# Optimization experiments

Measured on AMD Instinct MI355X. Metric: run time of the kernel, lower is better.

## Reference

```python
import jax, jax.numpy as jnp
import numpy as np
import math

B, S, D, H = 4, 1024, 1024, 16
HD = D // H  # 64
DFF = 4 * D
LN_EPS = 1e-5

def setup_inputs() -> dict:
    key = jax.random.key(0)
    ks = jax.random.split(key, 24)
    sd = lambda fi, fo: 1.0 / math.sqrt(fi)
    def lin(k, fi, fo):
        k1, k2 = jax.random.split(k)
        w = jax.random.uniform(k1, (fi, fo), jnp.float32, -sd(fi, fo), sd(fi, fo))
        b = jax.random.uniform(k2, (fo,), jnp.float32, -sd(fi, fo), sd(fi, fo))
        return w, b
    x = jax.random.normal(ks[0], (B, S, D), jnp.float32)
    Wk, bk = lin(ks[1], D, D)
    Wq, bq = lin(ks[2], D, D)
    Wv, bv = lin(ks[3], D, D)
    # per-head projections stacked over heads: [H, D, HD]
    def head_lin(k):
        kk = jax.random.split(k, H)
        ws, bs = zip(*[lin(kk[h], D, HD) for h in range(H)])
        return jnp.stack(ws), jnp.stack(bs)
    Whq, bhq = head_lin(ks[4])
    Whk, bhk = head_lin(ks[5])
    Whv, bhv = head_lin(ks[6])
    Wo, bo = lin(ks[7], D, D)
    W1, b1 = lin(ks[8], D, DFF)
    W2, b2 = lin(ks[9], DFF, D)
    gamma = jnp.ones((D,), jnp.float32)
    beta = jnp.zeros((D,), jnp.float32)
    return dict(x=x, Wk=Wk, bk=bk, Wq=Wq, bq=bq, Wv=Wv, bv=bv,
                Whq=Whq, bhq=bhq, Whk=Whk, bhk=bhk, Whv=Whv, bhv=bhv,
                Wo=Wo, bo=bo, W1=W1, b1=b1, W2=W2, b2=b2,
                gamma=gamma, beta=beta)

def _layer_norm(x, gamma, beta):
    mu = jnp.mean(x, axis=-1, keepdims=True)
    var = jnp.mean(jnp.square(x - mu), axis=-1, keepdims=True)
    return (x - mu) * jax.lax.rsqrt(var + LN_EPS) * gamma + beta

def reference(x, Wk, bk, Wq, bq, Wv, bv, Whq, bhq, Whk, bhk, Whv, bhv,
              Wo, bo, W1, b1, W2, b2, gamma, beta):
    # outer projections; NOTE: forward passes (k, q, v) into MHA, so the
    # MHA 'Q' stream is k_proj(x), 'K' stream is q_proj(x), 'V' is v_proj(x)
    ko = x @ Wk + bk
    qo = x @ Wq + bq
    vo = x @ Wv + bv
    # per-head projections (batched over heads): [B,H,S,HD]
    q = jnp.einsum('bsd,hde->bhse', ko, Whq) + bhq[None, :, None, :]
    k = jnp.einsum('bsd,hde->bhse', qo, Whk) + bhk[None, :, None, :]
    v = jnp.einsum('bsd,hde->bhse', vo, Whv) + bhv[None, :, None, :]
    # NOTE: original scales by sqrt(d_model), not sqrt(head_dim)
    scores = jnp.einsum('bhse,bhte->bhst', q, k) / math.sqrt(D)
    w = jax.nn.softmax(scores, axis=-1)
    o = jnp.einsum('bhst,bhte->bhse', w, v)         # [B,H,S,HD]
    o = o.transpose(0, 2, 1, 3).reshape(B, S, D)    # concat heads
    attn = o @ Wo + bo
    # dropout is identity in eval; shared LayerNorm after both residuals
    r1 = _layer_norm(x + attn, gamma, beta)
    ff = jax.nn.gelu(r1 @ W1 + b1, approximate=False) @ W2 + b2
    out = _layer_norm(r1 + ff, gamma, beta)
    return out
```

## Files before the change

### kernel.cpp

```cpp
#include <hip/hip_runtime.h>
#include <cstdint>
#include <cstddef>

#define D_MODEL 1024
#define SEQ 1024
#define BATCH 4
#define NHEAD 16
#define HDIM 64
#define ROWS (BATCH*SEQ)

typedef unsigned short u16;
typedef __attribute__((ext_vector_type(4))) unsigned short u16x4;
typedef __attribute__((ext_vector_type(8))) unsigned short u16x8;
typedef __attribute__((ext_vector_type(8))) __bf16 bf16x8v;
typedef __attribute__((ext_vector_type(4))) float f32x4;

__device__ inline u16 f2bf(float f){
  union{float f; unsigned u;} c; c.f = f;
  unsigned r = c.u + 0x7FFFu + ((c.u>>16)&1u);
  return (u16)(r>>16);
}
__device__ inline float bf2f(u16 s){
  union{unsigned u; float f;} c; c.u = ((unsigned)s)<<16; return c.f;
}
__device__ inline float gelu_f(float x){ return 0.5f*x*(1.f+erff(x*0.7071067811865475f)); }

__device__ __forceinline__ void gload_lds16(const void* g, void* l){
  __builtin_amdgcn_global_load_lds(
    (const __attribute__((address_space(1))) unsigned int*)g,
    (__attribute__((address_space(3))) unsigned int*)l, 16, 0, 0);
}

__global__ __launch_bounds__(256) void convert_bf(const float* __restrict__ in, u16* __restrict__ out){
  size_t idx = (size_t)blockIdx.x*256 + threadIdx.x;
  f32x4 v = *(const f32x4*)(in + idx*4);
  u16x4 o = { f2bf(v.x), f2bf(v.y), f2bf(v.z), f2bf(v.w) };
  *(u16x4*)(out + idx*4) = o;
}

__global__ __launch_bounds__(256) void transpose_conv(const float* __restrict__ W, u16* __restrict__ WT, int K, int N){
  __shared__ float tile[32][33];
  int n0 = blockIdx.x*32, k0 = blockIdx.y*32;
  int tx = threadIdx.x & 31, ty = threadIdx.x >> 5;
  #pragma unroll
  for (int i=0;i<4;i++){
    int r = ty + i*8;
    tile[r][tx] = W[(size_t)(k0+r)*N + n0 + tx];
  }
  __syncthreads();
  #pragma unroll
  for (int i=0;i<4;i++){
    int r = ty + i*8;
    WT[(size_t)(n0+r)*K + k0 + tx] = f2bf(tile[tx][r]);
  }
}

__global__ __launch_bounds__(256) void head_transpose(const float* __restrict__ Wh, u16* __restrict__ WT){
  __shared__ float tile[32][33];
  int d0 = blockIdx.x*32, e0 = blockIdx.y*32, h = blockIdx.z;
  int tx = threadIdx.x & 31, ty = threadIdx.x >> 5;
  #pragma unroll
  for (int i=0;i<4;i++){
    int r = ty + i*8;
    tile[r][tx] = Wh[(size_t)h*D_MODEL*HDIM + (size_t)(d0+r)*HDIM + e0 + tx];
  }
  __syncthreads();
  #pragma unroll
  for (int i=0;i<4;i++){
    int r = ty + i*8;
    WT[(size_t)(h*HDIM + e0 + r)*D_MODEL + d0 + tx] = f2bf(tile[tx][r]);
  }
}

__global__ __launch_bounds__(256) void bias_cat(const float* a, const float* b, const float* c, float* o){
  int i = blockIdx.x*256 + threadIdx.x;
  float v = (i < 1024) ? a[i] : (i < 2048) ? b[i-1024] : c[i-2048];
  o[i] = v;
}

__device__ __forceinline__ void stage128(u16 (*As)[4096], u16 (*Bs)[4096], int b,
  const u16* Ab, const u16* Bb, int Kstride, int kt, int wid, int rr, int sch)
{
  #pragma unroll
  for (int c=0;c<2;c++){
    int reg = c*4 + wid;
    int row = reg*16 + rr;
    gload_lds16(Ab + (size_t)row*Kstride + kt*32 + sch*8, &As[b][reg*512]);
  }
  #pragma unroll
  for (int c=0;c<2;c++){
    int reg = c*4 + wid;
    int row = reg*16 + rr;
    gload_lds16(Bb + (size_t)row*Kstride + kt*32 + sch*8, &Bs[b][reg*512]);
  }
}

__device__ __forceinline__ void gemm128_core(u16 (*As)[4096], u16 (*Bs)[4096],
  const u16* __restrict__ A, const u16* __restrict__ BT, const float* __restrict__ bias,
  float* __restrict__ outF, u16* __restrict__ outB,
  int N, int Kstride, int kofs, int Ksub, int mode, int act, int addbias)
{
  int t = threadIdx.x, lane = t&63, wid = t>>6;
  int wr = wid>>1, wc = wid&1;
  int fr = lane&15, kg = lane>>4;
  int gx = gridDim.x;
  int bid = blockIdx.y*gx + blockIdx.x;
  int nwg = gx*gridDim.y;
  int cpx = nwg >> 3;
  int sw = (bid&7)*cpx + (bid>>3);
  int tc = sw % gx, tr = sw / gx;

  const u16* Ab = A  + (size_t)tr*128*Kstride + kofs;
  const u16* Bb = BT + (size_t)tc*128*Kstride + kofs;
  int rr = lane>>2, cc = lane&3;
  int sch = cc ^ ((rr>>1)&3);

  f32x4 acc[4][4];
  #pragma unroll
  for (int m=0;m<4;m++)
    #pragma unroll
    for (int n=0;n<4;n++) acc[m][n] = (f32x4)0.f;

  int NT = Ksub >> 5;

  stage128(As, Bs, 0, Ab, Bb, Kstride, 0, wid, rr, sch);
  stage128(As, Bs, 1, Ab, Bb, Kstride, 1, wid, rr, sch);
  int buf = 0;
  for (int kt=0; kt<NT; ++kt){
    if (kt+2 < NT){
      int nb = buf+2; if (nb>=3) nb-=3;
      stage128(As, Bs, nb, Ab, Bb, Kstride, kt+2, wid, rr, sch);
      asm volatile("s_waitcnt vmcnt(8)" ::: "memory");
    } else if (kt+1 < NT){
      asm volatile("s_waitcnt vmcnt(4)" ::: "memory");
    } else {
      asm volatile("s_waitcnt vmcnt(0)" ::: "memory");
    }
    asm volatile("s_barrier" ::: "memory");
    bf16x8v af[4], bfv[4];
    #pragma unroll
    for (int m=0;m<4;m++){
      int r = wr*64 + m*16 + fr;
      af[m] = *(const bf16x8v*)&As[buf][r*32 + (kg ^ ((r>>1)&3))*8];
    }
    #pragma unroll
    for (int n=0;n<4;n++){
      int r = wc*64 + n*16 + fr;
      bfv[n] = *(const bf16x8v*)&Bs[buf][r*32 + (kg ^ ((r>>1)&3))*8];
    }
    #pragma unroll
    for (int m=0;m<4;m++)
      #pragma unroll
      for (int n=0;n<4;n++)
        acc[m][n] = __builtin_amdgcn_mfma_f32_16x16x32_bf16(af[m], bfv[n], acc[m][n], 0,0,0);
    if (kt+1 < NT)
      asm volatile("s_barrier" ::: "memory");
    buf += 1; if (buf >= 3) buf = 0;
  }

  int crow0 = tr*128 + wr*64;
  int ccol0 = tc*128 + wc*64;
  #pragma unroll
  for (int n=0;n<4;n++){
    int col = ccol0 + n*16 + fr;
    float bv = addbias ? bias[col] : 0.f;
    #pragma unroll
    for (int m=0;m<4;m++){
      int rbase = crow0 + m*16 + kg*4;
      #pragma unroll
      for (int i=0;i<4;i++){
        float v = acc[m][n][i] + bv;
        if (act) v = gelu_f(v);
        int row = rbase + i;
        if (mode == 0){
          outB[(size_t)(col>>10)*((size_t)ROWS*1024) + (size_t)row*1024 + (col&1023)] = f2bf(v);
        } else if (mode == 1){
          outB[(size_t)row*N + col] = f2bf(v);
        } else if (mode == 2){
          int b = row >> 10, s = row & 1023;
          int h = col >> 6, e = col & 63;
          outB[(((size_t)((b*NHEAD + h)*HDIM + e))<<10) + s] = f2bf(v);
        } else {
          outF[(size_t)row*1024 + col] = v;
        }
      }
    }
  }
}

__global__ __launch_bounds__(256) void g_gemm(
  const u16* A, const u16* BT, const float* bias, float* outF, u16* outB,
  int N, int K, int mode, int act)
{
  __shared__ __align__(16) u16 As[3][4096];
  __shared__ __align__(16) u16 Bs[3][4096];
  gemm128_core(As, Bs, A, BT, bias, outF, outB, N, K, 0, K, mode, act, 1);
}

__global__ __launch_bounds__(256) void g_gemm_sk(
  const u16* A, const u16* BT, const float* bias, float* outBase, int K)
{
  __shared__ __align__(16) u16 As[3][4096];
  __shared__ __align__(16) u16 Bs[3][4096];
  int z = blockIdx.z;
  int Ksub = K >> 1;
  gemm128_core(As, Bs, A, BT, bias, outBase + (size_t)z*ROWS*1024, nullptr,
               1024, K, z*Ksub, Ksub, 3, 0, z==0);
}

struct B3 { const u16* A[3]; const u16* BT[3]; const float* bias[3]; u16* Cb[3]; int mode[3]; };
__global__ __launch_bounds__(256) void g_gemm_b3(B3 p){
  __shared__ __align__(16) u16 As[3][4096];
  __shared__ __align__(16) u16 Bs[3][4096];
  int z = blockIdx.z;
  gemm128_core(As, Bs, p.A[z], p.BT[z], p.bias[z], nullptr, p.Cb[z],
               1024, 1024, 0, 1024, p.mode[z], 0, 1);
}

__global__ __launch_bounds__(256) void attn_mfma(const u16* __restrict__ Q, const u16* __restrict__ Km,
                                                 const u16* __restrict__ Vt, u16* __restrict__ O)
{
  __shared__ __align__(16) u16 Ks[64*64];
  __shared__ __align__(16) u16 Vs[64*64];
  __shared__ __align__(16) u16 Ps[4][16*64];
  int t = threadIdx.x, lane = t & 63, wid = t >> 6;
  int fr = lane & 15, kg = lane >> 4;
  int qt = blockIdx.x, h = blockIdx.y, b = blockIdx.z;
  const size_t qkbase = ((size_t)b*SEQ)*D_MODEL + (size_t)h*HDIM;
  const size_t vtb = ((size_t)(b*NHEAD + h))*HDIM*SEQ;

  int qrow = qt*64 + wid*16 + fr;
  bf16x8v aq[2];
  aq[0] = *(const bf16x8v*)(Q + qkbase + (size_t)qrow*D_MODEL + kg*8);
  aq[1] = *(const bf16x8v*)(Q + qkbase + (size_t)qrow*D_MODEL + 32 + kg*8);

  f32x4 Oacc[4];
  #pragma unroll
  for (int n=0;n<4;n++) Oacc[n] = (f32x4)0.f;
  float m_run[4], l_run[4];
  #pragma unroll
  for (int i=0;i<4;i++){ m_run[i] = -3e38f; l_run[i] = 0.f; }

  int srow = lane >> 3;
  int sch  = (lane & 7) ^ srow;
  int x7 = fr & 7;

  for (int kt = 0; kt < SEQ/64; ++kt){
    #pragma unroll
    for (int c=0;c<2;c++){
      int r0 = (wid*2 + c)*8;
      int rowk = r0 + srow;
      gload_lds16(Km + qkbase + (size_t)(kt*64 + rowk)*D_MODEL + sch*8, &Ks[r0*64]);
      gload_lds16(Vt + vtb + (size_t)rowk*SEQ + kt*64 + sch*8, &Vs[r0*64]);
    }
    __syncthreads();

    f32x4 z4 = (f32x4)0.f;
    f32x4 s4[4];
    #pragma unroll
    for (int n=0;n<4;n++){
      int r = n*16 + fr;
      bf16x8v k0v = *(const bf16x8v*)&Ks[r*64 + ((kg  ) ^ x7)*8];
      bf16x8v k1v = *(const bf16x8v*)&Ks[r*64 + ((4+kg) ^ x7)*8];
      s4[n] = __builtin_amdgcn_mfma_f32_16x16x32_bf16(aq[0], k0v, z4, 0,0,0);
      s4[n] = __builtin_amdgcn_mfma_f32_16x16x32_bf16(aq[1], k1v, s4[n], 0,0,0);
      s4[n] *= 0.03125f;
    }

    float mI[4], sc[4], ls[4], p[4][4];
    #pragma unroll
    for (int i=0;i<4;i++)
      mI[i] = fmaxf(fmaxf(s4[0][i], s4[1][i]), fmaxf(s4[2][i], s4[3][i]));
    #pragma unroll
    for (int off=1; off<16; off<<=1){
      #pragma unroll
      for (int i=0;i<4;i++) mI[i] = fmaxf(mI[i], __shfl_xor(mI[i], off));
    }
    #pragma unroll
    for (int i=0;i<4;i++){
      float m_new = fmaxf(m_run[i], mI[i]);
      sc[i] = __expf(m_run[i] - m_new);
      m_run[i] = m_new;
      ls[i] = 0.f;
    }
    #pragma unroll
    for (int n=0;n<4;n++)
      #pragma unroll
      for (int i=0;i<4;i++){
        float pv = __expf(s4[n][i] - m_run[i]);
        p[n][i] = pv;
        ls[i] += pv;
      }
    #pragma unroll
    for (int off=1; off<16; off<<=1){
      #pragma unroll
      for (int i=0;i<4;i++) ls[i] += __shfl_xor(ls[i], off);
    }
    #pragma unroll
    for (int i=0;i<4;i++) l_run[i] = l_run[i]*sc[i] + ls[i];
    #pragma unroll
    for (int n=0;n<4;n++)
      #pragma unroll
      for (int i=0;i<4;i++) Oacc[n][i] *= sc[i];

    u16* Pw = &Ps[wid][0];
    #pragma unroll
    for (int n=0;n<4;n++){
      int chunk = n*2 + (fr>>3);
      #pragma unroll
      for (int i=0;i<4;i++){
        int row = kg*4 + i;
        Pw[row*64 + (chunk ^ (row&7))*8 + (fr&7)] = f2bf(p[n][i]);
      }
    }
    asm volatile("s_waitcnt lgkmcnt(0)" ::: "memory");

    bf16x8v ap0 = *(const bf16x8v*)&Pw[fr*64 + ((kg  ) ^ x7)*8];
    bf16x8v ap1 = *(const bf16x8v*)&Pw[fr*64 + ((4+kg) ^ x7)*8];
    #pragma unroll
    for (int n2=0;n2<4;n2++){
      int r = n2*16 + fr;
      bf16x8v v0 = *(const bf16x8v*)&Vs[r*64 + ((kg  ) ^ x7)*8];
      bf16x8v v1 = *(const bf16x8v*)&Vs[r*64 + ((4+kg) ^ x7)*8];
      Oacc[n2] = __builtin_amdgcn_mfma_f32_16x16x32_bf16(ap0, v0, Oacc[n2], 0,0,0);
      Oacc[n2] = __builtin_amdgcn_mfma_f32_16x16x32_bf16(ap1, v1, Oacc[n2], 0,0,0);
    }
    __syncthreads();
  }

  float inv[4];
  #pragma unroll
  for (int i=0;i<4;i++) inv[i] = 1.f / l_run[i];
  #pragma unroll
  for (int n2=0;n2<4;n2++){
    #pragma unroll
    for (int i=0;i<4;i++){
      int row = qt*64 + wid*16 + kg*4 + i;
      O[qkbase + (size_t)row*D_MODEL + n2*16 + fr] = f2bf(Oacc[n2][i]*inv[i]);
    }
  }
}

__global__ __launch_bounds__(256) void ln_sum3(const float* __restrict__ A, const float* __restrict__ B,
   const float* __restrict__ C, const float* __restrict__ gamma, const float* __restrict__ beta,
   float* __restrict__ Of, u16* __restrict__ Ob)
{
  int row = blockIdx.x, t = threadIdx.x;
  size_t base = (size_t)row*D_MODEL + t*4;
  f32x4 v = *(const f32x4*)(A + base);
  v += *(const f32x4*)(B + base);
  v += *(const f32x4*)(C + base);
  float s = v.x+v.y+v.z+v.w;
  float q = v.x*v.x+v.y*v.y+v.z*v.z+v.w*v.w;
  #pragma unroll
  for (int off=1; off<64; off<<=1){ s += __shfl_xor(s,off); q += __shfl_xor(q,off); }
  __shared__ float red[8];
  int wid = t>>6;
  if ((t&63)==0){ red[wid] = s; red[wid+4] = q; }
  __syncthreads();
  s = red[0]+red[1]+red[2]+red[3];
  q = red[4]+red[5]+red[6]+red[7];
  float mu = s*(1.f/1024.f);
  float var = q*(1.f/1024.f) - mu*mu;
  float rs = rsqrtf(var + 1e-5f);
  f32x4 g4 = *(const f32x4*)(gamma + t*4);
  f32x4 b4 = *(const f32x4*)(beta + t*4);
  f32x4 o;
  o.x = (v.x-mu)*rs*g4.x + b4.x;
  o.y = (v.y-mu)*rs*g4.y + b4.y;
  o.z = (v.z-mu)*rs*g4.z + b4.z;
  o.w = (v.w-mu)*rs*g4.w + b4.w;
  if (Of) *(f32x4*)(Of + base) = o;
  if (Ob){
    u16x4 ob = { f2bf(o.x), f2bf(o.y), f2bf(o.z), f2bf(o.w) };
    *(u16x4*)(Ob + base) = ob;
  }
}

extern "C" void kernel_launch(void* const* d_in, const int* in_sizes, int n_in,
                              void* d_out, int out_size, void* d_ws, size_t ws_size,
                              hipStream_t stream)
{
  const float* x    = (const float*)d_in[0];
  const float* Wk   = (const float*)d_in[1];
  const float* bk   = (const float*)d_in[2];
  const float* Wq   = (const float*)d_in[3];
  const float* bq   = (const float*)d_in[4];
  const float* Wv   = (const float*)d_in[5];
  const float* bv   = (const float*)d_in[6];
  const float* Whq  = (const float*)d_in[7];
  const float* bhq  = (const float*)d_in[8];
  const float* Whk  = (const float*)d_in[9];
  const float* bhk  = (const float*)d_in[10];
  const float* Whv  = (const float*)d_in[11];
  const float* bhv  = (const float*)d_in[12];
  const float* Wo   = (const float*)d_in[13];
  const float* bo   = (const float*)d_in[14];
  const float* W1   = (const float*)d_in[15];
  const float* b1   = (const float*)d_in[16];
  const float* W2   = (const float*)d_in[17];
  const float* b2   = (const float*)d_in[18];
  const float* gamma= (const float*)d_in[19];
  const float* beta = (const float*)d_in[20];

  char* ws = (char*)d_ws;
  const size_t MB_ = 1024*1024;
  u16* WkT  = (u16*)(ws + 0*MB_);
  u16* WqT  = (u16*)(ws + 2*MB_);
  u16* WvT  = (u16*)(ws + 4*MB_);
  u16* WhqT = (u16*)(ws + 6*MB_);
  u16* WhkT = (u16*)(ws + 8*MB_);
  u16* WhvT = (u16*)(ws + 10*MB_);
  u16* WoT  = (u16*)(ws + 12*MB_);
  u16* W1T  = (u16*)(ws + 14*MB_);
  u16* W2T  = (u16*)(ws + 22*MB_);
  u16* xb   = (u16*)(ws + 30*MB_);
  u16* kob  = (u16*)(ws + 38*MB_);
  u16* qob  = (u16*)(ws + 46*MB_);
  u16* vob  = (u16*)(ws + 54*MB_);
  u16* qb   = (u16*)(ws + 62*MB_);
  u16* kb   = (u16*)(ws + 70*MB_);
  u16* vt   = (u16*)(ws + 78*MB_);
  u16* Ob   = (u16*)(ws + 86*MB_);
  u16* ff1b = (u16*)(ws + 38*MB_);
  float* r1f = (float*)(ws + 70*MB_);
  u16*  r1b  = (u16*)(ws + 86*MB_);
  float* P0  = (float*)(ws + 94*MB_);
  float* P1  = (float*)(ws + 110*MB_);
  float* bcat = (float*)(ws + 126*MB_);

  dim3 tb(256);

  convert_bf<<<dim3(ROWS*D_MODEL/4/256), tb, 0, stream>>>(x, xb);
  transpose_conv<<<dim3(32,32),  tb, 0, stream>>>(Wk, WkT, 1024, 1024);
  transpose_conv<<<dim3(32,32),  tb, 0, stream>>>(Wq, WqT, 1024, 1024);
  transpose_conv<<<dim3(32,32),  tb, 0, stream>>>(Wv, WvT, 1024, 1024);
  transpose_conv<<<dim3(32,32),  tb, 0, stream>>>(Wo, WoT, 1024, 1024);
  transpose_conv<<<dim3(128,32), tb, 0, stream>>>(W1, W1T, 1024, 4096);
  transpose_conv<<<dim3(32,128), tb, 0, stream>>>(W2, W2T, 4096, 1024);
  head_transpose<<<dim3(32,2,16), tb, 0, stream>>>(Whq, WhqT);
  head_transpose<<<dim3(32,2,16), tb, 0, stream>>>(Whk, WhkT);
  head_transpose<<<dim3(32,2,16), tb, 0, stream>>>(Whv, WhvT);
  bias_cat<<<dim3(12), tb, 0, stream>>>(bk, bq, bv, bcat);

  g_gemm<<<dim3(24,32), tb, 0, stream>>>(xb, WkT, bcat, nullptr, kob, 3072, 1024, 0, 0);

  B3 p2;
  p2.A[0]=kob; p2.A[1]=qob; p2.A[2]=vob;
  p2.BT[0]=WhqT; p2.BT[1]=WhkT; p2.BT[2]=WhvT;
  p2.bias[0]=bhq; p2.bias[1]=bhk; p2.bias[2]=bhv;
  p2.Cb[0]=qb; p2.Cb[1]=kb; p2.Cb[2]=vt;
  p2.mode[0]=1; p2.mode[1]=1; p2.mode[2]=2;
  g_gemm_b3<<<dim3(8,32,3), tb, 0, stream>>>(p2);

  attn_mfma<<<dim3(16,16,4), tb, 0, stream>>>(qb, kb, vt, Ob);

  g_gemm_sk<<<dim3(8,32,2), tb, 0, stream>>>(Ob, WoT, bo, P0, 1024);
  ln_sum3<<<dim3(4096), tb, 0, stream>>>(x, P0, P1, gamma, beta, r1f, r1b);
  g_gemm<<<dim3(32,32), tb, 0, stream>>>(r1b, W1T, b1, nullptr, ff1b, 4096, 1024, 1, 1);
  g_gemm_sk<<<dim3(8,32,2), tb, 0, stream>>>(ff1b, W2T, b2, P0, 4096);
  ln_sum3<<<dim3(4096), tb, 0, stream>>>(r1f, P0, P1, gamma, beta, (float*)d_out, nullptr);

  (void)in_sizes; (void)n_in; (void)out_size; (void)ws_size;
}
```

Measured before the change: 353.2 us.

## Replace 128x128 GEMM with 256x256 8-wave double-buffered kernel for QKV and FFN1

Adds a new GEMM kernel with 256x256 output tiles, 512 threads (8 waves), K-step 64 and XOR-swizzled LDS. It splits each K-step into four sub-phases that interleave global-to-LDS prefetch with MFMA work, and uses s_setprio around the MFMA bursts. Block IDs are remapped in an XCD-aware way. The kernel replaces the 128x128 kernel for the fused QKV projection and the first FFN GEMM, aiming for more operand reuse per LDS load and better overlap. The cost is fewer workgroups (192/256), which can under-fill the device's compute units, plus higher register pressure from 32 accumulators per lane.

```diff
diff --git a/kernel.cpp b/kernel.cpp
--- a/kernel.cpp
+++ b/kernel.cpp
@@ -76,6 +76,123 @@
   int i = blockIdx.x*256 + threadIdx.x;
   float v = (i < 1024) ? a[i] : (i < 2048) ? b[i-1024] : c[i-2048];
   o[i] = v;
+}
+
+__device__ __forceinline__ void phase16(const u16* Ah, const u16* Bh,
+  f32x4 acc[8][4], int mq, int nq, int wr, int wc, int fr, int kg)
+{
+  bf16x8v af[2][4], bfv[2][2];
+  #pragma unroll
+  for (int ks=0;ks<2;ks++){
+    #pragma unroll
+    for (int mf=0;mf<4;mf++){
+      int r = wr*64 + mf*16 + fr;
+      af[ks][mf] = *(const bf16x8v*)&Ah[r*64 + (((kg+4*ks)^(r&7)))*8];
+    }
+    #pragma unroll
+    for (int nf=0;nf<2;nf++){
+      int r = wc*32 + nf*16 + fr;
+      bfv[ks][nf] = *(const bf16x8v*)&Bh[r*64 + (((kg+4*ks)^(r&7)))*8];
+    }
+  }
+  __builtin_amdgcn_s_setprio(1);
+  #pragma unroll
+  for (int ks=0;ks<2;ks++)
+    #pragma unroll
+    for (int mf=0;mf<4;mf++)
+      #pragma unroll
+      for (int nf=0;nf<2;nf++)
+        acc[mq*4+mf][nq*2+nf] =
+          __builtin_amdgcn_mfma_f32_16x16x32_bf16(af[ks][mf], bfv[ks][nf], acc[mq*4+mf][nq*2+nf], 0,0,0);
+  __builtin_amdgcn_s_setprio(0);
+}
+
+__global__ __launch_bounds__(512,2) void gemm256_8p(
+  const u16* __restrict__ A, const u16* __restrict__ BT, const float* __restrict__ bias,
+  u16* __restrict__ outB, int N, int K, int mode, int act)
+{
+  __shared__ __align__(16) u16 As[2][2][128*64];
+  __shared__ __align__(16) u16 Bs[2][2][128*64];
+  int t = threadIdx.x, lane = t&63, wid = t>>6;
+  int wr = wid>>2, wc = wid&3;
+  int fr = lane&15, kg = lane>>4;
+  int gx = gridDim.x;
+  int bid = blockIdx.y*gx + blockIdx.x;
+  int nwg = gx*gridDim.y;
+  int cpx = nwg>>3;
+  int sw = (bid&7)*cpx + (bid>>3);
+  int tc = sw % gx, tr = sw / gx;
+
+  const u16* Abase = A  + (size_t)tr*256*K;
+  const u16* Bbase = BT + (size_t)tc*256*K;
+  int srow = lane>>3, sch8 = lane&7;
+
+  f32x4 acc[8][4];
+  #pragma unroll
+  for (int m=0;m<8;m++)
+    #pragma unroll
+    for (int n=0;n<4;n++) acc[m][n] = (f32x4)0.f;
+
+  #define STAGE_A8(buf,h,kt) { _Pragma("unroll") for (int li=0;li<2;li++){ \
+    int sr = (wid*2+li)*8 + srow; \
+    int gr = ((sr>>6)<<7) + (h)*64 + (sr&63); \
+    int sc = sch8 ^ (sr&7); \
+    gload_lds16(Abase + (size_t)gr*K + (size_t)(kt)*64 + sc*8, &As[buf][h][(wid*2+li)*512]); } }
+  #define STAGE_B8(buf,h,kt) { _Pragma("unroll") for (int li=0;li<2;li++){ \
+    int sr = (wid*2+li)*8 + srow; \
+    int gc = ((sr>>5)<<6) + (h)*32 + (sr&31); \
+    int sc = sch8 ^ (sr&7); \
+    gload_lds16(Bbase + (size_t)gc*K + (size_t)(kt)*64 + sc*8, &Bs[buf][h][(wid*2+li)*512]); } }
+  #define BAR asm volatile("s_barrier" ::: "memory")
+
+  int NT = K >> 6;
+  STAGE_A8(0,0,0); STAGE_B8(0,0,0); STAGE_B8(0,1,0); STAGE_A8(0,1,0);
+  asm volatile("s_waitcnt vmcnt(4)" ::: "memory");
+
+  for (int kt=0; kt<NT; ++kt){
+    int buf = kt&1, nb = buf^1;
+    int pre = (kt+1 < NT);
+    if (pre) STAGE_A8(nb,0,kt+1);
+    BAR;
+    phase16(&As[buf][0][0], &Bs[buf][0][0], acc, 0,0, wr,wc,fr,kg);
+    BAR;
+    if (pre){ STAGE_B8(nb,0,kt+1); asm volatile("s_waitcnt vmcnt(6)" ::: "memory"); }
+    else    { asm volatile("s_waitcnt vmcnt(2)" ::: "memory"); }
+    BAR;
+    phase16(&As[buf][0][0], &Bs[buf][1][0], acc, 0,1, wr,wc,fr,kg);
+    BAR;
+    if (pre){ STAGE_B8(nb,1,kt+1); asm volatile("s_waitcnt vmcnt(6)" ::: "memory"); }
+    else    { asm volatile("s_waitcnt vmcnt(0)" ::: "memory"); }
+    BAR;
+    phase16(&As[buf][1][0], &Bs[buf][0][0], acc, 1,0, wr,wc,fr,kg);
+    BAR;
+    if (pre){ STAGE_A8(nb,1,kt+1); asm volatile("s_waitcnt vmcnt(4)" ::: "memory"); }
+    BAR;
+    phase16(&As[buf][1][0], &Bs[buf][1][0], acc, 1,1, wr,wc,fr,kg);
+    BAR;
+  }
+
+  int crow0 = tr*256 + wr*128;
+  int ccol0 = tc*256 + wc*64;
+  #pragma unroll
+  for (int n=0;n<4;n++){
+    int col = ccol0 + n*16 + fr;
+    float bv = bias[mode==0 ? col : (col & (N-1))];
+    #pragma unroll
+    for (int m=0;m<8;m++){
+      int rbase = crow0 + m*16 + kg*4;
+      #pragma unroll
+      for (int i=0;i<4;i++){
+        float v = acc[m][n][i] + bv;
+        if (act) v = gelu_f(v);
+        int row = rbase + i;
+        if (mode == 0)
+          outB[(size_t)(col>>10)*((size_t)ROWS*1024) + (size_t)row*1024 + (col&1023)] = f2bf(v);
+        else
+          outB[(size_t)row*N + col] = f2bf(v);
+      }
+    }
+  }
 }
 
 __device__ __forceinline__ void stage128(u16 (*As)[4096], u16 (*Bs)[4096], int b,
@@ -186,15 +303,6 @@
       }
     }
   }
-}
-
-__global__ __launch_bounds__(256) void g_gemm(
-  const u16* A, const u16* BT, const float* bias, float* outF, u16* outB,
-  int N, int K, int mode, int act)
-{
-  __shared__ __align__(16) u16 As[3][4096];
-  __shared__ __align__(16) u16 Bs[3][4096];
-  gemm128_core(As, Bs, A, BT, bias, outF, outB, N, K, 0, K, mode, act, 1);
 }
 
 __global__ __launch_bounds__(256) void g_gemm_sk(
@@ -443,7 +551,7 @@
   head_transpose<<<dim3(32,2,16), tb, 0, stream>>>(Whv, WhvT);
   bias_cat<<<dim3(12), tb, 0, stream>>>(bk, bq, bv, bcat);
 
-  g_gemm<<<dim3(24,32), tb, 0, stream>>>(xb, WkT, bcat, nullptr, kob, 3072, 1024, 0, 0);
+  gemm256_8p<<<dim3(12,16), dim3(512), 0, stream>>>(xb, WkT, bcat, kob, 3072, 1024, 0, 0);
 
   B3 p2;
   p2.A[0]=kob; p2.A[1]=qob; p2.A[2]=vob;
@@ -457,7 +565,7 @@
 
   g_gemm_sk<<<dim3(8,32,2), tb, 0, stream>>>(Ob, WoT, bo, P0, 1024);
   ln_sum3<<<dim3(4096), tb, 0, stream>>>(x, P0, P1, gamma, beta, r1f, r1b);
-  g_gemm<<<dim3(32,32), tb, 0, stream>>>(r1b, W1T, b1, nullptr, ff1b, 4096, 1024, 1, 1);
+  gemm256_8p<<<dim3(16,16), dim3(512), 0, stream>>>(r1b, W1T, b1, ff1b, 4096, 1024, 1, 1);
   g_gemm_sk<<<dim3(8,32,2), tb, 0, stream>>>(ff1b, W2T, b2, P0, 4096);
   ln_sum3<<<dim3(4096), tb, 0, stream>>>(r1f, P0, P1, gamma, beta, (float*)d_out, nullptr);
 
```

New measurement: 371.9 us. 5.3% more time.
